# Kernel tuning notes

Hardware: AMD Instinct MI355X
Metric: run time of the kernel (lower is better)

The kernel has to match this reference:

```python
import jax, jax.numpy as jnp
import numpy as np

L = 2        # gnn_layers
D = 256      # hidden_dim
E = 1024     # emb_dim
NCLS = 7
NEG = 1e30


def lstm_cell(x, h, c, Wih, Whh, bih, bhh):
    # torch.nn.LSTMCell math; gate order i, f, g, o
    g = x @ Wih.T + bih + h @ Whh.T + bhh
    i, f, gg, o = jnp.split(g, 4, axis=-1)
    c2 = jax.nn.sigmoid(f) * c + jax.nn.sigmoid(i) * jnp.tanh(gg)
    return jax.nn.sigmoid(o) * jnp.tanh(c2), c2


def dag_layer(Hl, adj_f, W1, W2, Wr, Wc_ih, Wc_hh, bc_ih, bc_hh, Wp_ih, Wp_hh, bp_ih, bp_hh):
    # Hl: (B,N,D). Sequential DAG recurrence with dot-product attention over growing prefix.
    B, N, Dh = Hl.shape
    zeros = jnp.zeros((B, Dh), Hl.dtype)
    h0 = Hl[:, 0]
    C0, _ = lstm_cell(h0, zeros, zeros, Wc_ih, Wc_hh, bc_ih, bc_hh)
    P0, _ = lstm_cell(zeros, h0, h0, Wp_ih, Wp_hh, bp_ih, bp_hh)
    Ht0 = C0 + P0
    # carry pre-projected keys/values incrementally to avoid O(N^2 D^2) work
    K2 = jnp.zeros((B, N, Dh), Hl.dtype).at[:, 0].set(Ht0 @ W2.T)
    Vr = jnp.zeros((B, N, Dh), Hl.dtype).at[:, 0].set(Ht0 @ Wr.T)
    H1 = jnp.zeros((B, N, Dh), Hl.dtype).at[:, 0].set(Ht0)
    pos = jnp.arange(N)

    def step(carry, i):
        K2, Vr, H1 = carry
        Q = jax.lax.dynamic_index_in_dim(Hl, i, axis=1, keepdims=False)      # (B,D)
        adj_i = jax.lax.dynamic_index_in_dim(adj_f, i, axis=1, keepdims=False)  # (B,N)
        q = Q @ W1.T
        logits = jnp.einsum('bd,bnd->bn', q, K2) - (1.0 - adj_i) * NEG  # mask_logic
        logits = jnp.where(pos[None, :] < i, logits, -NEG)              # only prefix :i
        w = jax.nn.softmax(logits, axis=-1)
        M = jnp.einsum('bn,bnd->bd', w, Vr)
        C, _ = lstm_cell(Q, M, M, Wc_ih, Wc_hh, bc_ih, bc_hh)
        P, _ = lstm_cell(M, Q, Q, Wp_ih, Wp_hh, bp_ih, bp_hh)
        Ht = C + P
        K2 = K2.at[:, i].set(Ht @ W2.T)
        Vr = Vr.at[:, i].set(Ht @ Wr.T)
        H1 = H1.at[:, i].set(Ht)
        return (K2, Vr, H1), None

    (K2, Vr, H1), _ = jax.lax.scan(step, (K2, Vr, H1), jnp.arange(1, N))
    return H1


def setup_inputs() -> dict:
    key = jax.random.key(0)
    ks = iter(jax.random.split(key, 40))
    B, N = 16, 128
    s = lambda *sh: jax.random.normal(next(ks), sh, jnp.float32) * 0.02
    in_dim = D * (L + 1) + E
    return dict(
        features=jax.random.normal(next(ks), (B, N, E), jnp.float32),
        adj=jnp.ones((B, N, N), jnp.int32),
        s_mask=jnp.zeros((B, N, N), jnp.int32),
        s_mask_onehot=jnp.zeros((B, N, N, 2), jnp.int32),
        lengths=jnp.ones((B,), jnp.int32) * N,
        fc1_W=s(D, E), fc1_b=jnp.zeros((D,), jnp.float32),
        W1=s(L, D, D), W2=s(L, D, D), Wr=s(L, D, D),
        Wc_ih=s(L, 4 * D, D), Wc_hh=s(L, 4 * D, D),
        bc_ih=jnp.zeros((L, 4 * D), jnp.float32), bc_hh=jnp.zeros((L, 4 * D), jnp.float32),
        Wp_ih=s(L, 4 * D, D), Wp_hh=s(L, 4 * D, D),
        bp_ih=jnp.zeros((L, 4 * D), jnp.float32), bp_hh=jnp.zeros((L, 4 * D), jnp.float32),
        m0_W=s(D, in_dim), m0_b=jnp.zeros((D,), jnp.float32),
        m1_W=s(D, D), m1_b=jnp.zeros((D,), jnp.float32),
        m2_W=s(NCLS, D), m2_b=jnp.zeros((NCLS,), jnp.float32),
    )


def reference(features, adj, s_mask, s_mask_onehot, lengths,
              fc1_W, fc1_b, W1, W2, Wr,
              Wc_ih, Wc_hh, bc_ih, bc_hh,
              Wp_ih, Wp_hh, bp_ih, bp_hh,
              m0_W, m0_b, m1_W, m1_b, m2_W, m2_b):
    # s_mask / s_mask_onehot unused for attn_type='dotprod', no_rel_attn=True
    # lengths unused for nodal_att_type=None (attentive_node_features is identity)
    adj_f = adj.astype(features.dtype)
    H0 = jax.nn.relu(features @ fc1_W.T + fc1_b)
    Hs = [H0]
    for l in range(L):
        Hs.append(dag_layer(Hs[l], adj_f,
                            W1[l], W2[l], Wr[l],
                            Wc_ih[l], Wc_hh[l], bc_ih[l], bc_hh[l],
                            Wp_ih[l], Wp_hh[l], bp_ih[l], bp_hh[l]))
    Hcat = jnp.concatenate(Hs + [features], axis=2)  # (B,N,D*(L+1)+E)
    h = jax.nn.relu(Hcat @ m0_W.T + m0_b)
    h = jax.nn.relu(h @ m1_W.T + m1_b)  # mlp_layers-1 extra layer; dropout p=0 -> identity
    return h @ m2_W.T + m2_b            # (B,N,num_class)
```

## Files before the change

### kernel.cpp

```cpp
#include <hip/hip_runtime.h>
#include <math.h>

#define B_ 16
#define N_ 128
#define D_ 256
#define E_ 1024
#define GD4 1024

template<bool BIAS, bool RELU>
__global__ __launch_bounds__(256) void gemm_k(const float* __restrict__ X,
    const float* __restrict__ W, const float* __restrict__ bias,
    float* __restrict__ C, int M, int N, int K)
{
  __shared__ float Xs[32][68];
  __shared__ float Ws[32][68];
  const int tid = threadIdx.x;
  const int m0 = blockIdx.x * 64, n0 = blockIdx.y * 64;
  const int tm = tid >> 4, tn = tid & 15;
  float acc[4][4] = {};
  for (int k0 = 0; k0 < K; k0 += 32) {
    for (int e = tid; e < 2048; e += 256) {
      int mm = e >> 5, kk = e & 31;
      Xs[kk][mm] = X[(m0+mm)*K + k0+kk];
    }
    for (int e = tid; e < 2048; e += 256) {
      int nn = e >> 5, kk = e & 31;
      Ws[kk][nn] = (n0+nn < N) ? W[(n0+nn)*K + k0+kk] : 0.f;
    }
    __syncthreads();
    for (int kk = 0; kk < 32; kk++) {
      float4 a = *(const float4*)&Xs[kk][tm*4];
      float4 b = *(const float4*)&Ws[kk][tn*4];
      acc[0][0] += a.x*b.x; acc[0][1] += a.x*b.y; acc[0][2] += a.x*b.z; acc[0][3] += a.x*b.w;
      acc[1][0] += a.y*b.x; acc[1][1] += a.y*b.y; acc[1][2] += a.y*b.z; acc[1][3] += a.y*b.w;
      acc[2][0] += a.z*b.x; acc[2][1] += a.z*b.y; acc[2][2] += a.z*b.z; acc[2][3] += a.z*b.w;
      acc[3][0] += a.w*b.x; acc[3][1] += a.w*b.y; acc[3][2] += a.w*b.z; acc[3][3] += a.w*b.w;
    }
    __syncthreads();
  }
  for (int i2 = 0; i2 < 4; i2++) {
    int row = m0 + tm*4 + i2;
    for (int j2 = 0; j2 < 4; j2++) {
      int col = n0 + tn*4 + j2;
      if (col < N) {
        float v = acc[i2][j2];
        if (BIAS) v += bias[col];
        if (RELU) v = fmaxf(v, 0.f);
        C[row*N + col] = v;
      }
    }
  }
}

__global__ __launch_bounds__(256) void prepamat_k(const float* __restrict__ W2,
    const float* __restrict__ W1, float* __restrict__ AM)
{
  __shared__ float Xs[32][68];
  __shared__ float Ws[32][68];
  const int tid = threadIdx.x;
  const int m0 = blockIdx.x * 64, n0 = blockIdx.y * 64;
  const float* X = W2 + blockIdx.z * 65536;
  const float* W = W1 + blockIdx.z * 65536;
  float* C = AM + blockIdx.z * 65536;
  const int tm = tid >> 4, tn = tid & 15;
  float acc[4][4] = {};
  for (int k0 = 0; k0 < 256; k0 += 32) {
    for (int e = tid; e < 2048; e += 256) {
      int kk = e >> 6, mm = e & 63;
      Xs[kk][mm] = X[(k0+kk)*256 + m0+mm];
    }
    for (int e = tid; e < 2048; e += 256) {
      int kk = e >> 6, nn = e & 63;
      Ws[kk][nn] = W[(k0+kk)*256 + n0+nn];
    }
    __syncthreads();
    for (int kk = 0; kk < 32; kk++) {
      float4 a = *(const float4*)&Xs[kk][tm*4];
      float4 b = *(const float4*)&Ws[kk][tn*4];
      acc[0][0] += a.x*b.x; acc[0][1] += a.x*b.y; acc[0][2] += a.x*b.z; acc[0][3] += a.x*b.w;
      acc[1][0] += a.y*b.x; acc[1][1] += a.y*b.y; acc[1][2] += a.y*b.z; acc[1][3] += a.y*b.w;
      acc[2][0] += a.z*b.x; acc[2][1] += a.z*b.y; acc[2][2] += a.z*b.z; acc[2][3] += a.z*b.w;
      acc[3][0] += a.w*b.x; acc[3][1] += a.w*b.y; acc[3][2] += a.w*b.z; acc[3][3] += a.w*b.w;
    }
    __syncthreads();
  }
  for (int i2 = 0; i2 < 4; i2++)
    for (int j2 = 0; j2 < 4; j2++)
      C[(m0 + tm*4 + i2)*256 + n0 + tn*4 + j2] = acc[i2][j2];
}

__global__ __launch_bounds__(256) void prepnn_k(const float* __restrict__ Wch,
    const float* __restrict__ Wpi, const float* __restrict__ Wr,
    float* __restrict__ OUT)
{
  __shared__ float Xs[32][68];
  __shared__ float Ws[32][68];
  const int tid = threadIdx.x;
  const int m0 = blockIdx.x * 64, n0 = blockIdx.y * 64;
  const int l = blockIdx.z;
  const float* X = (m0 < 1024) ? (Wch + l*262144 + m0*256)
                               : (Wpi + l*262144 + (m0-1024)*256);
  const float* W = Wr + l*65536;
  float* C = OUT + l*524288;
  const int tm = tid >> 4, tn = tid & 15;
  float acc[4][4] = {};
  for (int k0 = 0; k0 < 256; k0 += 32) {
    for (int e = tid; e < 2048; e += 256) {
      int mm = e >> 5, kk = e & 31;
      Xs[kk][mm] = X[mm*256 + k0+kk];
    }
    for (int e = tid; e < 2048; e += 256) {
      int kk = e >> 6, nn = e & 63;
      Ws[kk][nn] = W[(k0+kk)*256 + n0+nn];
    }
    __syncthreads();
    for (int kk = 0; kk < 32; kk++) {
      float4 a = *(const float4*)&Xs[kk][tm*4];
      float4 b = *(const float4*)&Ws[kk][tn*4];
      acc[0][0] += a.x*b.x; acc[0][1] += a.x*b.y; acc[0][2] += a.x*b.z; acc[0][3] += a.x*b.w;
      acc[1][0] += a.y*b.x; acc[1][1] += a.y*b.y; acc[1][2] += a.y*b.z; acc[1][3] += a.y*b.w;
      acc[2][0] += a.z*b.x; acc[2][1] += a.z*b.y; acc[2][2] += a.z*b.z; acc[2][3] += a.z*b.w;
      acc[3][0] += a.w*b.x; acc[3][1] += a.w*b.y; acc[3][2] += a.w*b.z; acc[3][3] += a.w*b.w;
    }
    __syncthreads();
  }
  for (int i2 = 0; i2 < 4; i2++)
    for (int j2 = 0; j2 < 4; j2++)
      C[(m0 + tm*4 + i2)*256 + n0 + tn*4 + j2] = acc[i2][j2];
}

__global__ void bias_sum_k(const float* __restrict__ bci, const float* __restrict__ bch,
                           const float* __restrict__ bpi, const float* __restrict__ bph,
                           float* __restrict__ bcC, float* __restrict__ bpC)
{
  int i = blockIdx.x*256 + threadIdx.x;
  if (i < 2048) { bcC[i] = bci[i] + bch[i]; bpC[i] = bpi[i] + bph[i]; }
}

__global__ void pack_k(const float* __restrict__ wchpi, const float* __restrict__ wr,
                       float* __restrict__ out)
{
  int idx = blockIdx.x*256 + threadIdx.x;
  int l  = idx / 589824; int r2 = idx % 589824;
  int sl = r2 / 36864;   int rem = r2 % 36864;
  int r  = rem / 4096;   int rem2 = rem % 4096;
  int o  = rem2 >> 10;   int t = (rem2 >> 2) & 255; int j = rem2 & 3;
  int d  = sl*16 + (t >> 4);
  int c  = (t & 15)*16 + o*4 + j;
  float v;
  if (r < 8) v = wchpi[l*524288 + (r*256 + d)*256 + c];
  else       v = wr[l*65536 + d*256 + c];
  out[idx] = v;
}

__global__ __launch_bounds__(256) void prologue_k(const float* __restrict__ X,
    const float* __restrict__ Wc, const float* __restrict__ Wp,
    const float* __restrict__ Am, const float* __restrict__ bcc,
    const float* __restrict__ bpc, float* __restrict__ GQC,
    float* __restrict__ GQP, float* __restrict__ VM)
{
  __shared__ float Xs[32][68];
  __shared__ float Ws[32][68];
  const int tid = threadIdx.x;
  const int m0 = blockIdx.x * 64;
  const int nt = blockIdx.y;
  const float* W; const float* bias; float* C; int n0; int NC;
  if (nt < 16)      { W = Wc; bias = bcc;     C = GQC; n0 = nt*64;      NC = 1024; }
  else if (nt < 32) { W = Wp; bias = bpc;     C = GQP; n0 = (nt-16)*64; NC = 1024; }
  else              { W = Am; bias = nullptr; C = VM;  n0 = (nt-32)*64; NC = 256;  }
  const int tm = tid >> 4, tn = tid & 15;
  float acc[4][4] = {};
  for (int k0 = 0; k0 < 256; k0 += 32) {
    for (int e = tid; e < 2048; e += 256) {
      int mm = e >> 5, kk = e & 31;
      Xs[kk][mm] = X[(m0+mm)*256 + k0+kk];
    }
    for (int e = tid; e < 2048; e += 256) {
      int nn = e >> 5, kk = e & 31;
      Ws[kk][nn] = W[(n0+nn)*256 + k0+kk];
    }
    __syncthreads();
    for (int kk = 0; kk < 32; kk++) {
      float4 a = *(const float4*)&Xs[kk][tm*4];
      float4 b = *(const float4*)&Ws[kk][tn*4];
      acc[0][0] += a.x*b.x; acc[0][1] += a.x*b.y; acc[0][2] += a.x*b.z; acc[0][3] += a.x*b.w;
      acc[1][0] += a.y*b.x; acc[1][1] += a.y*b.y; acc[1][2] += a.y*b.z; acc[1][3] += a.y*b.w;
      acc[2][0] += a.z*b.x; acc[2][1] += a.z*b.y; acc[2][2] += a.z*b.z; acc[2][3] += a.z*b.w;
      acc[3][0] += a.w*b.x; acc[3][1] += a.w*b.y; acc[3][2] += a.w*b.z; acc[3][3] += a.w*b.w;
    }
    __syncthreads();
  }
  for (int i2 = 0; i2 < 4; i2++) {
    int row = m0 + tm*4 + i2;
    for (int j2 = 0; j2 < 4; j2++) {
      int col = n0 + tn*4 + j2;
      float v = acc[i2][j2];
      if (bias) v += bias[col];
      C[row*NC + col] = v;
    }
  }
}

__global__ __launch_bounds__(256) void m0fused_k(const float* __restrict__ H0,
    const float* __restrict__ H1, const float* __restrict__ H2,
    const float* __restrict__ feat, const float* __restrict__ W,
    const float* __restrict__ bias, float* __restrict__ C)
{
  __shared__ float Xs[32][68];
  __shared__ float Ws[32][68];
  const int tid = threadIdx.x;
  const int m0 = blockIdx.x * 64, n0 = blockIdx.y * 64;
  const int tm = tid >> 4, tn = tid & 15;
  float acc[4][4] = {};
  for (int k0 = 0; k0 < 1792; k0 += 32) {
    for (int e = tid; e < 2048; e += 256) {
      int mm = e >> 5, kk = e & 31;
      int k = k0 + kk, row = m0 + mm;
      float v;
      if (k < 768) {
        const float* src = (k < 256) ? H0 : ((k < 512) ? H1 : H2);
        v = src[row*256 + (k & 255)];
      } else v = feat[row*1024 + (k - 768)];
      Xs[kk][mm] = v;
    }
    for (int e = tid; e < 2048; e += 256) {
      int nn = e >> 5, kk = e & 31;
      Ws[kk][nn] = W[(n0+nn)*1792 + k0+kk];
    }
    __syncthreads();
    for (int kk = 0; kk < 32; kk++) {
      float4 a = *(const float4*)&Xs[kk][tm*4];
      float4 b = *(const float4*)&Ws[kk][tn*4];
      acc[0][0] += a.x*b.x; acc[0][1] += a.x*b.y; acc[0][2] += a.x*b.z; acc[0][3] += a.x*b.w;
      acc[1][0] += a.y*b.x; acc[1][1] += a.y*b.y; acc[1][2] += a.y*b.z; acc[1][3] += a.y*b.w;
      acc[2][0] += a.z*b.x; acc[2][1] += a.z*b.y; acc[2][2] += a.z*b.z; acc[2][3] += a.z*b.w;
      acc[3][0] += a.w*b.x; acc[3][1] += a.w*b.y; acc[3][2] += a.w*b.z; acc[3][3] += a.w*b.w;
    }
    __syncthreads();
  }
  for (int i2 = 0; i2 < 4; i2++) {
    int row = m0 + tm*4 + i2;
    for (int j2 = 0; j2 < 4; j2++) {
      int col = n0 + tn*4 + j2;
      C[row*256 + col] = fmaxf(acc[i2][j2] + bias[col], 0.f);
    }
  }
}

__device__ __forceinline__ float sigf(float x) { return 1.f / (1.f + __expf(-x)); }
__device__ __forceinline__ float tanhfast(float x) {
  float xc = fminf(fmaxf(x, -15.f), 15.f);
  float e = __expf(-2.f * xc);
  return (1.f - e) / (1.f + e);
}

__global__ __launch_bounds__(512) void scan_k(
    const float* __restrict__ Hl,
    const float* __restrict__ Vm,
    const float* __restrict__ gqC,
    const float* __restrict__ gqP,
    const float* __restrict__ WTp,
    const int*   __restrict__ adj,
    float* __restrict__ Hout,
    unsigned* __restrict__ cnt)
{
  __shared__ float4 wl4[9216];
  __shared__ float s_lds[256];
  __shared__ float v_s[256];
  __shared__ float ssum[2][256];
  __shared__ float psum[128];
  __shared__ float aw[128];
  __shared__ int   adj_s[128];
  __shared__ float gqc_l[64];
  __shared__ float gqp_l[64];
  __shared__ float gsum[9][16];
  __shared__ float ql[16];
  __shared__ float red[4];

  const int tid = threadIdx.x;
  const int b   = blockIdx.x >> 4;
  const int sl  = blockIdx.x & 15;
  unsigned* mycnt = cnt + b*32;

  { const float4* src = (const float4*)WTp + sl*9216;
    for (int e = tid; e < 9216; e += 512) wl4[e] = src[e]; }

  const int rr = tid >> 2;
  const int rj = tid & 3;
  const int th = tid >> 8;
  const int t8 = tid & 255;

  for (int i = 0; i < N_; ++i) {
    __syncthreads();
    if (tid < 256)       v_s[tid] = Vm[(b*N_ + i)*D_ + tid];
    else if (tid < 320)  { int u = tid-256; gqc_l[u] = gqC[(b*N_+i)*GD4 + (u>>4)*D_ + sl*16 + (u&15)]; }
    else if (tid < 384)  { int u = tid-320; gqp_l[u] = gqP[(b*N_+i)*GD4 + (u>>4)*D_ + sl*16 + (u&15)]; }
    else                 { int u = tid-384; adj_s[u] = adj[(b*N_ + i)*N_ + u]; }
    if (tid < 16) ql[tid] = Hl[(b*N_+i)*D_ + sl*16 + tid];

    if (i > 0) {
      if (tid == 0) {
        unsigned tgt = 16u * (unsigned)i;
        while (__hip_atomic_load(mycnt, __ATOMIC_RELAXED, __HIP_MEMORY_SCOPE_AGENT) < tgt)
          __builtin_amdgcn_s_sleep(1);
      }
      __syncthreads();
      asm volatile("" ::: "memory");

      {
        float acc = 0.f;
        if (rr < i) {
          const float4* hp = (const float4*)(Hout + ((size_t)(b*N_ + rr))*D_) + rj;
          const float4* vv = (const float4*)v_s + rj;
          #pragma unroll
          for (int c4 = 0; c4 < 16; ++c4) {
            float4 a = hp[c4*4];
            float4 w = vv[c4*4];
            acc += a.x*w.x + a.y*w.y + a.z*w.z + a.w*w.w;
          }
        }
        acc += __shfl_xor(acc, 1, 64);
        acc += __shfl_xor(acc, 2, 64);
        if (rj == 0) psum[rr] = acc;
      }
      __syncthreads();

      float lg = -1e30f;
      if (tid < 128) {
        lg = ((tid < i) && (adj_s[tid] != 0)) ? psum[tid] : -1e30f;
        float mv = lg;
        for (int off = 32; off >= 1; off >>= 1) mv = fmaxf(mv, __shfl_xor(mv, off, 64));
        if ((tid & 63) == 0) red[tid >> 6] = mv;
      }
      __syncthreads();
      if (tid < 128) {
        float mx = fmaxf(red[0], red[1]);
        float ev = (lg > -1e29f) ? __expf(lg - mx) : 0.f;
        aw[tid] = ev;
        float sv = ev;
        for (int off = 32; off >= 1; off >>= 1) sv += __shfl_xor(sv, off, 64);
        if ((tid & 63) == 0) red[2 + (tid >> 6)] = sv;
      }
      __syncthreads();

      {
        const float* hb = Hout + (size_t)b*N_*D_ + t8;
        int k0 = th ? (i >> 1) : 0;
        int k1 = th ? i : (i >> 1);
        float s0=0.f, s1=0.f, s2=0.f, s3=0.f;
        int kk = k0;
        for (; kk + 4 <= k1; kk += 4) {
          s0 += aw[kk+0] * hb[(kk+0)*D_];
          s1 += aw[kk+1] * hb[(kk+1)*D_];
          s2 += aw[kk+2] * hb[(kk+2)*D_];
          s3 += aw[kk+3] * hb[(kk+3)*D_];
        }
        for (; kk < k1; ++kk) s0 += aw[kk] * hb[kk*D_];
        ssum[th][t8] = (s0+s1) + (s2+s3);
      }
      __syncthreads();
      if (tid < 256) {
        float inv = 1.f / (red[2] + red[3]);
        s_lds[tid] = (ssum[0][tid] + ssum[1][tid]) * inv;
      }
      __syncthreads();
    } else {
      __syncthreads();
      if (tid < 256) s_lds[tid] = 0.f;
      __syncthreads();
    }

    {
      float4 sv0 = *(const float4*)&s_lds[(t8 & 15)*16 + 0];
      float4 sv1 = *(const float4*)&s_lds[(t8 & 15)*16 + 4];
      float4 sv2 = *(const float4*)&s_lds[(t8 & 15)*16 + 8];
      float4 sv3 = *(const float4*)&s_lds[(t8 & 15)*16 + 12];
      float g0=0.f, g1=0.f, g2=0.f, g3=0.f, g4=0.f;
      #define ROWDOT(r) ({                                                   \
        float4 w0 = wl4[((r)*4+0)*256 + t8];                                 \
        float4 w1 = wl4[((r)*4+1)*256 + t8];                                 \
        float4 w2 = wl4[((r)*4+2)*256 + t8];                                 \
        float4 w3 = wl4[((r)*4+3)*256 + t8];                                 \
        w0.x*sv0.x + w0.y*sv0.y + w0.z*sv0.z + w0.w*sv0.w                    \
      + w1.x*sv1.x + w1.y*sv1.y + w1.z*sv1.z + w1.w*sv1.w                    \
      + w2.x*sv2.x + w2.y*sv2.y + w2.z*sv2.z + w2.w*sv2.w                    \
      + w3.x*sv3.x + w3.y*sv3.y + w3.z*sv3.z + w3.w*sv3.w; })
      if (th == 0) { g0 = ROWDOT(0); g1 = ROWDOT(1); g2 = ROWDOT(2); g3 = ROWDOT(3); }
      else         { g0 = ROWDOT(4); g1 = ROWDOT(5); g2 = ROWDOT(6); g3 = ROWDOT(7); g4 = ROWDOT(8); }
      #undef ROWDOT
      #pragma unroll
      for (int m = 1; m <= 8; m <<= 1) {
        g0 += __shfl_xor(g0, m, 64);
        g1 += __shfl_xor(g1, m, 64);
        g2 += __shfl_xor(g2, m, 64);
        g3 += __shfl_xor(g3, m, 64);
        g4 += __shfl_xor(g4, m, 64);
      }
      if ((t8 & 15) == 0) {
        int d = t8 >> 4;
        if (th == 0) { gsum[0][d]=g0; gsum[1][d]=g1; gsum[2][d]=g2; gsum[3][d]=g3; }
        else         { gsum[4][d]=g0; gsum[5][d]=g1; gsum[6][d]=g2; gsum[7][d]=g3; gsum[8][d]=g4; }
      }
    }
    __syncthreads();

    if (tid < 16) {
      int dl = tid;
      float Mv = gsum[8][dl];
      float Qv = ql[dl];
      float giC = gsum[0][dl] + gqc_l[ 0 + dl];
      float gfC = gsum[1][dl] + gqc_l[16 + dl];
      float ggC = gsum[2][dl] + gqc_l[32 + dl];
      float goC = gsum[3][dl] + gqc_l[48 + dl];
      float giP = gsum[4][dl] + gqp_l[ 0 + dl];
      float gfP = gsum[5][dl] + gqp_l[16 + dl];
      float ggP = gsum[6][dl] + gqp_l[32 + dl];
      float goP = gsum[7][dl] + gqp_l[48 + dl];
      float c2C = sigf(gfC)*Mv + sigf(giC)*tanhfast(ggC);
      float Cv  = sigf(goC)*tanhfast(c2C);
      float c2P = sigf(gfP)*Qv + sigf(giP)*tanhfast(ggP);
      float Pv  = sigf(goP)*tanhfast(c2P);
      float htv = Cv + Pv;
      int d = sl*16 + dl;
      __hip_atomic_store(&Hout[(b*N_ + i)*D_ + d], htv,
                         __ATOMIC_RELAXED, __HIP_MEMORY_SCOPE_AGENT);
    }

    __syncthreads();
    if (tid == 0) {
      asm volatile("s_waitcnt vmcnt(0)" ::: "memory");
      __hip_atomic_fetch_add(mycnt, 1u, __ATOMIC_RELAXED, __HIP_MEMORY_SCOPE_AGENT);
    }
  }
}

extern "C" void kernel_launch(void* const* d_in, const int* in_sizes, int n_in,
                              void* d_out, int out_size, void* d_ws, size_t ws_size,
                              hipStream_t stream)
{
  const float* features = (const float*)d_in[0];
  const int*   adj      = (const int*)  d_in[1];
  const float* fc1_W    = (const float*)d_in[5];
  const float* fc1_b    = (const float*)d_in[6];
  const float* W1       = (const float*)d_in[7];
  const float* W2       = (const float*)d_in[8];
  const float* Wr       = (const float*)d_in[9];
  const float* Wc_ih    = (const float*)d_in[10];
  const float* Wc_hh    = (const float*)d_in[11];
  const float* bc_ih    = (const float*)d_in[12];
  const float* bc_hh    = (const float*)d_in[13];
  const float* Wp_ih    = (const float*)d_in[14];
  const float* Wp_hh    = (const float*)d_in[15];
  const float* bp_ih    = (const float*)d_in[16];
  const float* bp_hh    = (const float*)d_in[17];
  const float* m0_W     = (const float*)d_in[18];
  const float* m0_b     = (const float*)d_in[19];
  const float* m1_W     = (const float*)d_in[20];
  const float* m1_b     = (const float*)d_in[21];
  const float* m2_W     = (const float*)d_in[22];
  const float* m2_b     = (const float*)d_in[23];

  float* ws = (float*)d_ws;
  float* WTP    = ws + 0;
  float* AMAT   = ws + 1179648;
  float* BCC    = ws + 1310720;
  float* BPC    = ws + 1312768;
  float* WCHPI  = ws + 1314816;
  float* H0     = ws + 2363392;
  float* H1     = ws + 2887680;
  float* H2     = ws + 3411968;
  float* VMAT   = ws + 3936256;
  float* GQC    = ws + 4460544;
  float* GQP    = ws + 6557696;
  unsigned* CNT = (unsigned*)(ws + 8654848);
  float* HB1    = ws + 8655872;
  float* HB2    = ws + 9180160;

  hipMemsetAsync(CNT, 0, 4096, stream);
  bias_sum_k<<<8, 256, 0, stream>>>(bc_ih, bc_hh, bp_ih, bp_hh, BCC, BPC);
  prepamat_k<<<dim3(4,4,2), 256, 0, stream>>>(W2, W1, AMAT);
  prepnn_k<<<dim3(32,4,2), 256, 0, stream>>>(Wc_hh, Wp_ih, Wr, WCHPI);
  pack_k<<<4608, 256, 0, stream>>>(WCHPI, Wr, WTP);

  gemm_k<true,true><<<dim3(32,4), 256, 0, stream>>>(features, fc1_W, fc1_b, H0, 2048, 256, 1024);

  prologue_k<<<dim3(32,36), 256, 0, stream>>>(H0, Wc_ih, Wp_hh, AMAT,
                                              BCC, BPC, GQC, GQP, VMAT);
  scan_k<<<256, 512, 0, stream>>>(H0, VMAT, GQC, GQP, WTP, adj, H1, CNT);

  prologue_k<<<dim3(32,36), 256, 0, stream>>>(H1, Wc_ih + 262144, Wp_hh + 262144,
                                              AMAT + 65536, BCC + 1024, BPC + 1024,
                                              GQC, GQP, VMAT);
  scan_k<<<256, 512, 0, stream>>>(H1, VMAT, GQC, GQP, WTP + 589824, adj, H2, CNT + 512);

  m0fused_k<<<dim3(32,4), 256, 0, stream>>>(H0, H1, H2, features, m0_W, m0_b, HB1);
  gemm_k<true,true ><<<dim3(32,4), 256, 0, stream>>>(HB1, m1_W, m1_b, HB2, 2048, 256, 256);
  gemm_k<true,false><<<dim3(32,1), 256, 0, stream>>>(HB2, m2_W, m2_b, (float*)d_out, 2048, 7, 256);
}
```

Before: 2.024 ms.

## Use per-block flag slots, prefetch prior rows before the wait, and drop the softmax max pass

Replaces the single shared counter per batch with one counter slot per (batch, slice) block, polled by 16 threads, which avoids atomic contention on one address. Rows completed before the previous step are loaded into registers before the spin-wait, and only the newest row is read after it, so memory latency overlaps the synchronisation. The softmax drops its max subtraction and the two reduction barriers, and the normalising sum is folded into the weighted-sum loop. The weight packing and the s_lds indexing change so vector loads are contiguous, and the trailing barrier is removed. Skipping the max shift risks overflow if the logits grow large, and the workspace offsets move to make room for the larger counter array.

```diff
diff --git a/kernel.cpp b/kernel.cpp
--- a/kernel.cpp
+++ b/kernel.cpp
@@ -146,7 +146,7 @@
   int r  = rem / 4096;   int rem2 = rem % 4096;
   int o  = rem2 >> 10;   int t = (rem2 >> 2) & 255; int j = rem2 & 3;
   int d  = sl*16 + (t >> 4);
-  int c  = (t & 15)*16 + o*4 + j;
+  int c  = o*64 + (t & 15)*4 + j;
   float v;
   if (r < 8) v = wchpi[l*524288 + (r*256 + d)*256 + c];
   else       v = wr[l*65536 + d*256 + c];
@@ -267,7 +267,7 @@
   __shared__ float4 wl4[9216];
   __shared__ float s_lds[256];
   __shared__ float v_s[256];
-  __shared__ float ssum[2][256];
+  __shared__ float ssum[2][257];
   __shared__ float psum[128];
   __shared__ float aw[128];
   __shared__ int   adj_s[128];
@@ -275,12 +275,11 @@
   __shared__ float gqp_l[64];
   __shared__ float gsum[9][16];
   __shared__ float ql[16];
-  __shared__ float red[4];
 
   const int tid = threadIdx.x;
   const int b   = blockIdx.x >> 4;
   const int sl  = blockIdx.x & 15;
-  unsigned* mycnt = cnt + b*32;
+  unsigned* myslot = cnt + (b*16 + sl)*32;
 
   { const float4* src = (const float4*)WTp + sl*9216;
     for (int e = tid; e < 9216; e += 512) wl4[e] = src[e]; }
@@ -299,22 +298,30 @@
     if (tid < 16) ql[tid] = Hl[(b*N_+i)*D_ + sl*16 + tid];
 
     if (i > 0) {
-      if (tid == 0) {
-        unsigned tgt = 16u * (unsigned)i;
-        while (__hip_atomic_load(mycnt, __ATOMIC_RELAXED, __HIP_MEMORY_SCOPE_AGENT) < tgt)
+      float4 areg[16];
+      const float4* hp = (const float4*)(Hout + ((size_t)(b*N_ + rr))*D_) + rj;
+      if (rr + 1 < i) {
+        #pragma unroll
+        for (int c4 = 0; c4 < 16; ++c4) areg[c4] = hp[c4*4];
+      }
+      if (tid < 16) {
+        unsigned* slot = cnt + (b*16 + tid)*32;
+        while (__hip_atomic_load(slot, __ATOMIC_RELAXED, __HIP_MEMORY_SCOPE_AGENT) < (unsigned)i)
           __builtin_amdgcn_s_sleep(1);
       }
       __syncthreads();
       asm volatile("" ::: "memory");
-
+      if (rr + 1 == i) {
+        #pragma unroll
+        for (int c4 = 0; c4 < 16; ++c4) areg[c4] = hp[c4*4];
+      }
       {
         float acc = 0.f;
         if (rr < i) {
-          const float4* hp = (const float4*)(Hout + ((size_t)(b*N_ + rr))*D_) + rj;
           const float4* vv = (const float4*)v_s + rj;
           #pragma unroll
           for (int c4 = 0; c4 < 16; ++c4) {
-            float4 a = hp[c4*4];
+            float4 a = areg[c4];
             float4 w = vv[c4*4];
             acc += a.x*w.x + a.y*w.y + a.z*w.z + a.w*w.w;
           }
@@ -325,84 +332,73 @@
       }
       __syncthreads();
 
-      float lg = -1e30f;
-      if (tid < 128) {
-        lg = ((tid < i) && (adj_s[tid] != 0)) ? psum[tid] : -1e30f;
-        float mv = lg;
-        for (int off = 32; off >= 1; off >>= 1) mv = fmaxf(mv, __shfl_xor(mv, off, 64));
-        if ((tid & 63) == 0) red[tid >> 6] = mv;
-      }
-      __syncthreads();
-      if (tid < 128) {
-        float mx = fmaxf(red[0], red[1]);
-        float ev = (lg > -1e29f) ? __expf(lg - mx) : 0.f;
-        aw[tid] = ev;
-        float sv = ev;
-        for (int off = 32; off >= 1; off >>= 1) sv += __shfl_xor(sv, off, 64);
-        if ((tid & 63) == 0) red[2 + (tid >> 6)] = sv;
-      }
+      if (tid < 128)
+        aw[tid] = ((tid < i) && (adj_s[tid] != 0)) ? __expf(psum[tid]) : 0.f;
       __syncthreads();
 
       {
         const float* hb = Hout + (size_t)b*N_*D_ + t8;
         int k0 = th ? (i >> 1) : 0;
         int k1 = th ? i : (i >> 1);
-        float s0=0.f, s1=0.f, s2=0.f, s3=0.f;
+        float s0=0.f, s1=0.f, s2=0.f, s3=0.f, z=0.f;
         int kk = k0;
         for (; kk + 4 <= k1; kk += 4) {
-          s0 += aw[kk+0] * hb[(kk+0)*D_];
-          s1 += aw[kk+1] * hb[(kk+1)*D_];
-          s2 += aw[kk+2] * hb[(kk+2)*D_];
-          s3 += aw[kk+3] * hb[(kk+3)*D_];
+          float a0=aw[kk+0], a1=aw[kk+1], a2=aw[kk+2], a3=aw[kk+3];
+          z  += (a0+a1)+(a2+a3);
+          s0 += a0 * hb[(kk+0)*D_];
+          s1 += a1 * hb[(kk+1)*D_];
+          s2 += a2 * hb[(kk+2)*D_];
+          s3 += a3 * hb[(kk+3)*D_];
         }
-        for (; kk < k1; ++kk) s0 += aw[kk] * hb[kk*D_];
+        for (; kk < k1; ++kk) { float a=aw[kk]; z+=a; s0 += a*hb[kk*D_]; }
         ssum[th][t8] = (s0+s1) + (s2+s3);
+        if (t8 == 0) ssum[th][256] = z;
       }
       __syncthreads();
       if (tid < 256) {
-        float inv = 1.f / (red[2] + red[3]);
+        float inv = 1.f / (ssum[0][256] + ssum[1][256]);
         s_lds[tid] = (ssum[0][tid] + ssum[1][tid]) * inv;
       }
       __syncthreads();
+
+      {
+        const float4* s4 = (const float4*)s_lds;
+        float4 sv0 = s4[ 0 + (t8 & 15)];
+        float4 sv1 = s4[16 + (t8 & 15)];
+        float4 sv2 = s4[32 + (t8 & 15)];
+        float4 sv3 = s4[48 + (t8 & 15)];
+        float g0=0.f, g1=0.f, g2=0.f, g3=0.f, g4=0.f;
+        #define ROWDOT(r) ({                                                 \
+          float4 w0 = wl4[((r)*4+0)*256 + t8];                               \
+          float4 w1 = wl4[((r)*4+1)*256 + t8];                               \
+          float4 w2 = wl4[((r)*4+2)*256 + t8];                               \
+          float4 w3 = wl4[((r)*4+3)*256 + t8];                               \
+          w0.x*sv0.x + w0.y*sv0.y + w0.z*sv0.z + w0.w*sv0.w                  \
+        + w1.x*sv1.x + w1.y*sv1.y + w1.z*sv1.z + w1.w*sv1.w                  \
+        + w2.x*sv2.x + w2.y*sv2.y + w2.z*sv2.z + w2.w*sv2.w                  \
+        + w3.x*sv3.x + w3.y*sv3.y + w3.z*sv3.z + w3.w*sv3.w; })
+        if (th == 0) { g0 = ROWDOT(0); g1 = ROWDOT(1); g2 = ROWDOT(2); g3 = ROWDOT(3); }
+        else         { g0 = ROWDOT(4); g1 = ROWDOT(5); g2 = ROWDOT(6); g3 = ROWDOT(7); g4 = ROWDOT(8); }
+        #undef ROWDOT
+        #pragma unroll
+        for (int m = 1; m <= 8; m <<= 1) {
+          g0 += __shfl_xor(g0, m, 64);
+          g1 += __shfl_xor(g1, m, 64);
+          g2 += __shfl_xor(g2, m, 64);
+          g3 += __shfl_xor(g3, m, 64);
+          g4 += __shfl_xor(g4, m, 64);
+        }
+        if ((t8 & 15) == 0) {
+          int d = t8 >> 4;
+          if (th == 0) { gsum[0][d]=g0; gsum[1][d]=g1; gsum[2][d]=g2; gsum[3][d]=g3; }
+          else         { gsum[4][d]=g0; gsum[5][d]=g1; gsum[6][d]=g2; gsum[7][d]=g3; gsum[8][d]=g4; }
+        }
+      }
+      __syncthreads();
     } else {
-      __syncthreads();
-      if (tid < 256) s_lds[tid] = 0.f;
-      __syncthreads();
-    }
-
-    {
-      float4 sv0 = *(const float4*)&s_lds[(t8 & 15)*16 + 0];
-      float4 sv1 = *(const float4*)&s_lds[(t8 & 15)*16 + 4];
-      float4 sv2 = *(const float4*)&s_lds[(t8 & 15)*16 + 8];
-      float4 sv3 = *(const float4*)&s_lds[(t8 & 15)*16 + 12];
-      float g0=0.f, g1=0.f, g2=0.f, g3=0.f, g4=0.f;
-      #define ROWDOT(r) ({                                                   \
-        float4 w0 = wl4[((r)*4+0)*256 + t8];                                 \
-        float4 w1 = wl4[((r)*4+1)*256 + t8];                                 \
-        float4 w2 = wl4[((r)*4+2)*256 + t8];                                 \
-        float4 w3 = wl4[((r)*4+3)*256 + t8];                                 \
-        w0.x*sv0.x + w0.y*sv0.y + w0.z*sv0.z + w0.w*sv0.w                    \
-      + w1.x*sv1.x + w1.y*sv1.y + w1.z*sv1.z + w1.w*sv1.w                    \
-      + w2.x*sv2.x + w2.y*sv2.y + w2.z*sv2.z + w2.w*sv2.w                    \
-      + w3.x*sv3.x + w3.y*sv3.y + w3.z*sv3.z + w3.w*sv3.w; })
-      if (th == 0) { g0 = ROWDOT(0); g1 = ROWDOT(1); g2 = ROWDOT(2); g3 = ROWDOT(3); }
-      else         { g0 = ROWDOT(4); g1 = ROWDOT(5); g2 = ROWDOT(6); g3 = ROWDOT(7); g4 = ROWDOT(8); }
-      #undef ROWDOT
-      #pragma unroll
-      for (int m = 1; m <= 8; m <<= 1) {
-        g0 += __shfl_xor(g0, m, 64);
-        g1 += __shfl_xor(g1, m, 64);
-        g2 += __shfl_xor(g2, m, 64);
-        g3 += __shfl_xor(g3, m, 64);
-        g4 += __shfl_xor(g4, m, 64);
-      }
-      if ((t8 & 15) == 0) {
-        int d = t8 >> 4;
-        if (th == 0) { gsum[0][d]=g0; gsum[1][d]=g1; gsum[2][d]=g2; gsum[3][d]=g3; }
-        else         { gsum[4][d]=g0; gsum[5][d]=g1; gsum[6][d]=g2; gsum[7][d]=g3; gsum[8][d]=g4; }
-      }
-    }
-    __syncthreads();
+      if (tid < 144) gsum[tid >> 4][tid & 15] = 0.f;
+      __syncthreads();
+    }
 
     if (tid < 16) {
       int dl = tid;
@@ -425,11 +421,9 @@
       __hip_atomic_store(&Hout[(b*N_ + i)*D_ + d], htv,
                          __ATOMIC_RELAXED, __HIP_MEMORY_SCOPE_AGENT);
     }
-
-    __syncthreads();
     if (tid == 0) {
       asm volatile("s_waitcnt vmcnt(0)" ::: "memory");
-      __hip_atomic_fetch_add(mycnt, 1u, __ATOMIC_RELAXED, __HIP_MEMORY_SCOPE_AGENT);
+      __hip_atomic_fetch_add(myslot, 1u, __ATOMIC_RELAXED, __HIP_MEMORY_SCOPE_AGENT);
     }
   }
 }
@@ -473,10 +467,10 @@
   float* GQC    = ws + 4460544;
   float* GQP    = ws + 6557696;
   unsigned* CNT = (unsigned*)(ws + 8654848);
-  float* HB1    = ws + 8655872;
-  float* HB2    = ws + 9180160;
-
-  hipMemsetAsync(CNT, 0, 4096, stream);
+  float* HB1    = ws + 8671232;
+  float* HB2    = ws + 9195520;
+
+  hipMemsetAsync(CNT, 0, 65536, stream);
   bias_sum_k<<<8, 256, 0, stream>>>(bc_ih, bc_hh, bp_ih, bp_hh, BCC, BPC);
   prepamat_k<<<dim3(4,4,2), 256, 0, stream>>>(W2, W1, AMAT);
   prepnn_k<<<dim3(32,4,2), 256, 0, stream>>>(Wc_hh, Wp_ih, Wr, WCHPI);
@@ -491,7 +485,7 @@
   prologue_k<<<dim3(32,36), 256, 0, stream>>>(H1, Wc_ih + 262144, Wp_hh + 262144,
                                               AMAT + 65536, BCC + 1024, BPC + 1024,
                                               GQC, GQP, VMAT);
-  scan_k<<<256, 512, 0, stream>>>(H1, VMAT, GQC, GQP, WTP + 589824, adj, H2, CNT + 512);
+  scan_k<<<256, 512, 0, stream>>>(H1, VMAT, GQC, GQP, WTP + 589824, adj, H2, CNT + 8192);
 
   m0fused_k<<<dim3(32,4), 256, 0, stream>>>(H0, H1, H2, features, m0_W, m0_b, HB1);
   gemm_k<true,true ><<<dim3(32,4), 256, 0, stream>>>(HB1, m1_W, m1_b, HB2, 2048, 256, 256);
```

Result: faster. 1.976 ms (-2.4%).
